# Kernel tuning notes

Hardware: AMD Instinct MI355X
Metric: run time of the kernel (lower is better)

Reference implementation:

```python
import jax, jax.numpy as jnp
import numpy as np

N, D, Z, T, K = 100000, 128, 128, 1024, 256
HID = 512
D_IN = D + 2 * Z  # concat of ctx, z_ctx_pe, z_tgt_pe


def setup_inputs() -> dict:
    key = jax.random.key(0)
    ks = jax.random.split(key, 12)
    inp = {
        'pe': jax.random.normal(ks[0], (N, 4), jnp.float32),
        'context_embedding': jax.random.normal(ks[1], (N, D), jnp.float32),
        'target_embedding': jax.random.normal(ks[2], (N, D), jnp.float32),
        # padded 2-hop subgraph node ids per target (precomputed k_hop_subgraph)
        'sub_nodes': jax.random.randint(ks[3], (T, K), 0, N, jnp.int32),
        'sub_counts': jax.random.randint(ks[4], (T,), 1, K + 1, jnp.int32),
        'target_nodes': jax.random.randint(ks[5], (T,), 0, N, jnp.int32),
        # params
        'z': jax.random.normal(ks[6], (1, Z), jnp.float32) * 0.1,
        'W_pe': jax.random.normal(ks[7], (4, Z), jnp.float32) * 0.5,
        'W1': jax.random.normal(ks[8], (D_IN, HID), jnp.float32) * (1.0 / np.sqrt(D_IN)),
        'b1': jnp.zeros((HID,), jnp.float32),
        'W2': jax.random.normal(ks[9], (HID, D), jnp.float32) * (1.0 / np.sqrt(HID)),
        'b2': jnp.zeros((D,), jnp.float32),
    }
    return inp


def reference(pe, context_embedding, target_embedding, sub_nodes, sub_counts,
              target_nodes, z, W_pe, W1, b1, W2, b2):
    # position_encoding = pe_projector(laplacian_eigenvector_pe)  [N, Z]
    pos_enc = pe @ W_pe
    # gather per-subgraph quantities (batched over T targets, padded to K)
    sub_ctx = context_embedding[sub_nodes]            # [T, K, D]
    z_ctx_pe = z + pos_enc[sub_nodes]                 # [T, K, Z]
    z_tgt_pe = z + pos_enc[target_nodes][:, None, :]  # [T, 1, Z] -> broadcast
    z_tgt_pe = jnp.broadcast_to(z_tgt_pe, z_ctx_pe.shape)
    agg = jnp.concatenate([sub_ctx, z_ctx_pe, z_tgt_pe], axis=-1)  # [T, K, D_IN]
    # predictor MLP
    pred = jax.nn.relu(agg @ W1 + b1) @ W2 + b2       # [T, K, D]
    tgt = target_embedding[target_nodes][:, None, :]  # [T, 1, D]
    sq = (pred - tgt) ** 2                            # [T, K, D]
    counts = jnp.maximum(sub_counts, 1)
    mask = (jnp.arange(K)[None, :] < counts[:, None]).astype(sq.dtype)  # [T, K]
    # per-target MSELoss (mean over n_sub * D elements), summed over targets
    per_target = jnp.sum(sq * mask[:, :, None], axis=(1, 2)) / (counts.astype(sq.dtype) * D)
    return jnp.sum(per_target)
```

## Files before the change

kernel.cpp:

```cpp
#include <hip/hip_runtime.h>
#include <hip/hip_bf16.h>

#define NN   100000
#define DD   128
#define ZZ   128
#define TT   1024
#define KK   256
#define HIDD 512

typedef __attribute__((ext_vector_type(8))) short  short8;
typedef __attribute__((ext_vector_type(4))) float  f32x4;

__device__ inline unsigned short f2bf(float f) {
    union { float f; unsigned int u; } x; x.f = f;
    unsigned int r = x.u + 0x7fffu + ((x.u >> 16) & 1u);
    return (unsigned short)(r >> 16);
}
__device__ inline void load_lds16(const void* g, void* l) {
    __builtin_amdgcn_global_load_lds((const __attribute__((address_space(1))) unsigned int*)g,
                                     (__attribute__((address_space(3))) unsigned int*)l, 16, 0, 0);
}

__global__ __launch_bounds__(256) void prep_tables(
    const float* __restrict__ pe, const float* __restrict__ ctx,
    const float* __restrict__ z, const float* __restrict__ wpe,
    unsigned short* __restrict__ ctx_bf, unsigned short* __restrict__ zpe_bf) {
    int g = blockIdx.x * 256 + threadIdx.x;
    if (g >= NN * 16) return;
    int n = g >> 4, j8 = (g & 15) << 3;
    float p0 = pe[n * 4 + 0], p1 = pe[n * 4 + 1], p2 = pe[n * 4 + 2], p3 = pe[n * 4 + 3];
    float4 c0 = *(const float4*)(ctx + (size_t)n * 128 + j8);
    float4 c1 = *(const float4*)(ctx + (size_t)n * 128 + j8 + 4);
    float4 z0 = *(const float4*)(z + j8);
    float4 z1 = *(const float4*)(z + j8 + 4);
    float4 wa0 = *(const float4*)(wpe + 0 * ZZ + j8), wa1 = *(const float4*)(wpe + 0 * ZZ + j8 + 4);
    float4 wb0 = *(const float4*)(wpe + 1 * ZZ + j8), wb1 = *(const float4*)(wpe + 1 * ZZ + j8 + 4);
    float4 wc0 = *(const float4*)(wpe + 2 * ZZ + j8), wc1 = *(const float4*)(wpe + 2 * ZZ + j8 + 4);
    float4 wd0 = *(const float4*)(wpe + 3 * ZZ + j8), wd1 = *(const float4*)(wpe + 3 * ZZ + j8 + 4);
    float zp[8], cv[8];
    zp[0] = z0.x + p0 * wa0.x + p1 * wb0.x + p2 * wc0.x + p3 * wd0.x;
    zp[1] = z0.y + p0 * wa0.y + p1 * wb0.y + p2 * wc0.y + p3 * wd0.y;
    zp[2] = z0.z + p0 * wa0.z + p1 * wb0.z + p2 * wc0.z + p3 * wd0.z;
    zp[3] = z0.w + p0 * wa0.w + p1 * wb0.w + p2 * wc0.w + p3 * wd0.w;
    zp[4] = z1.x + p0 * wa1.x + p1 * wb1.x + p2 * wc1.x + p3 * wd1.x;
    zp[5] = z1.y + p0 * wa1.y + p1 * wb1.y + p2 * wc1.y + p3 * wd1.y;
    zp[6] = z1.z + p0 * wa1.z + p1 * wb1.z + p2 * wc1.z + p3 * wd1.z;
    zp[7] = z1.w + p0 * wa1.w + p1 * wb1.w + p2 * wc1.w + p3 * wd1.w;
    cv[0] = c0.x; cv[1] = c0.y; cv[2] = c0.z; cv[3] = c0.w;
    cv[4] = c1.x; cv[5] = c1.y; cv[6] = c1.z; cv[7] = c1.w;
    short8 sz, sc;
#pragma unroll
    for (int i = 0; i < 8; ++i) { sz[i] = (short)f2bf(zp[i]); sc[i] = (short)f2bf(cv[i]); }
    *(short8*)(zpe_bf + (size_t)g * 8) = sz;
    *(short8*)(ctx_bf + (size_t)g * 8) = sc;
}

__global__ __launch_bounds__(256) void pack_ct(
    const float* __restrict__ W1, const float* __restrict__ W2,
    const float* __restrict__ pe, const float* __restrict__ z, const float* __restrict__ wpe,
    const int* __restrict__ target_nodes, const float* __restrict__ b1,
    unsigned short* __restrict__ w1p, unsigned short* __restrict__ w2p, float* __restrict__ ct_g) {
    __shared__ float zp[8][128];
    int tid = threadIdx.x;
    if (blockIdx.x < 768) {
        int g = blockIdx.x * 256 + tid;
        if (g < 256 * HIDD) {
            int e = g & 7, l = (g >> 3) & 63, tile = g >> 9;
            int ntg = tile & 7, rem = tile >> 3;
            int kc = rem & 7, hc = rem >> 3;
            int k = kc * 32 + (l >> 4) * 8 + e;
            int n = hc * 128 + ntg * 16 + (l & 15);
            w1p[g] = f2bf(W1[(size_t)k * HIDD + n]);
        } else {
            int q = g - 256 * HIDD;
            int e = q & 7, l = (q >> 3) & 63, tile = q >> 9;
            int ntg = tile & 7, kcg = tile >> 3;
            int k = kcg * 32 + (l >> 4) * 8 + e;
            int n = ntg * 16 + (l & 15);
            w2p[q] = f2bf(W2[(size_t)k * DD + n]);
        }
        return;
    }
    int b = blockIdx.x - 768;
#pragma unroll
    for (int q = 0; q < 4; ++q) {
        int idx = q * 256 + tid;
        int t8 = idx >> 7, zz = idx & 127;
        int tgt = target_nodes[b * 8 + t8];
        zp[t8][zz] = z[zz] + pe[tgt * 4 + 0] * wpe[zz] + pe[tgt * 4 + 1] * wpe[128 + zz]
                           + pe[tgt * 4 + 2] * wpe[256 + zz] + pe[tgt * 4 + 3] * wpe[384 + zz];
    }
    __syncthreads();
    int j0 = tid, j1 = tid + 256;
    float a0[8], a1[8];
    float bb0 = b1[j0], bb1 = b1[j1];
#pragma unroll
    for (int t8 = 0; t8 < 8; ++t8) { a0[t8] = bb0; a1[t8] = bb1; }
#pragma unroll 8
    for (int zz = 0; zz < 128; ++zz) {
        float w0 = W1[(size_t)(256 + zz) * HIDD + j0];
        float w1 = W1[(size_t)(256 + zz) * HIDD + j1];
#pragma unroll
        for (int t8 = 0; t8 < 8; ++t8) { a0[t8] += zp[t8][zz] * w0; a1[t8] += zp[t8][zz] * w1; }
    }
#pragma unroll
    for (int t8 = 0; t8 < 8; ++t8) {
        ct_g[(size_t)(b * 8 + t8) * HIDD + j0] = a0[t8];
        ct_g[(size_t)(b * 8 + t8) * HIDD + j1] = a1[t8];
    }
}

__global__ __launch_bounds__(512) void mp_jepa_main(
    const unsigned short* __restrict__ ctx_bf,
    const unsigned short* __restrict__ zpe_bf,
    const unsigned short* __restrict__ w1p,
    const unsigned short* __restrict__ w2p,
    const float* __restrict__ ct_g,
    const float* __restrict__ target_embedding,
    const int* __restrict__ sub_nodes,
    const int* __restrict__ sub_counts,
    const int* __restrict__ target_nodes,
    const float* __restrict__ b2,
    float* __restrict__ out) {
    const int bid = blockIdx.x;
    const int kt = bid >> 10, t = bid & 1023;
    const int k0 = kt * 64;
    int cnt = sub_counts[t]; if (cnt < 1) cnt = 1;
    if (k0 >= cnt) return;
    const int tgt = target_nodes[t];

    __shared__ __align__(16) unsigned short ctxT[64 * 128];
    __shared__ __align__(16) unsigned short zpeT[64 * 128];
    __shared__ __align__(16) unsigned short hT[64 * 128];
    __shared__ float cts[HIDD];
    __shared__ float tgte[DD];
    __shared__ float b2s[DD];
    __shared__ float red[8];

    const int tid = threadIdx.x;
    const int w = tid >> 6, l = tid & 63;
    const int wm = w & 1, wn = w >> 1;
    const int lo = l & 15, hi = l >> 4;

    {
        const char* cc = (const char*)ctx_bf;
        const char* zc = (const char*)zpe_bf;
        const int base = t * KK + k0;
#pragma unroll
        for (int it = 0; it < 2; ++it) {
            int rgrp = it * 32 + (w << 2);
            int row  = rgrp + hi;
            int node = sub_nodes[base + row];
            int soff = (lo << 4) ^ ((row & 7) << 4);
            load_lds16(cc + (size_t)node * 256 + soff, (char*)ctxT + rgrp * 256);
            load_lds16(zc + (size_t)node * 256 + soff, (char*)zpeT + rgrp * 256);
        }
    }
    if (tid < 128) {
        tgte[tid] = target_embedding[(size_t)tgt * 128 + tid];
        b2s[tid]  = b2[tid];
    }
    cts[tid] = ct_g[(size_t)t * HIDD + tid];
    __syncthreads();

    const short8* w1v = (const short8*)w1p;
    const short8* w2v = (const short8*)w2p;

    f32x4 accP[2][2];
#pragma unroll
    for (int rg = 0; rg < 2; ++rg)
#pragma unroll
        for (int nt = 0; nt < 2; ++nt) accP[rg][nt] = (f32x4){0.f, 0.f, 0.f, 0.f};

    for (int hc = 0; hc < 4; ++hc) {
        f32x4 acc1[2][2];
#pragma unroll
        for (int nt = 0; nt < 2; ++nt) {
            f32x4 cv = *(const f32x4*)&cts[(hc << 7) + (((wn << 1) + nt) << 4) + (hi << 2)];
            acc1[0][nt] = cv;
            acc1[1][nt] = cv;
        }
#pragma unroll
        for (int kc = 0; kc < 8; ++kc) {
            short8 bf0 = w1v[((((hc << 3) + kc) << 3) + (wn << 1) + 0) * 64 + l];
            short8 bf1 = w1v[((((hc << 3) + kc) << 3) + (wn << 1) + 1) * 64 + l];
            const unsigned short* src = (kc < 4) ? ctxT : zpeT;
            int cb = ((kc & 3) << 6) + (hi << 4);
            short8 a[2];
#pragma unroll
            for (int rg = 0; rg < 2; ++rg) {
                int row = (wm << 5) + (rg << 4) + lo;
                a[rg] = *(const short8*)(src + ((row * 256 + (cb ^ ((row & 7) << 4))) >> 1));
            }
#pragma unroll
            for (int rg = 0; rg < 2; ++rg) {
                acc1[rg][0] = __builtin_amdgcn_mfma_f32_16x16x32_bf16(bf0, a[rg], acc1[rg][0], 0, 0, 0);
                acc1[rg][1] = __builtin_amdgcn_mfma_f32_16x16x32_bf16(bf1, a[rg], acc1[rg][1], 0, 0, 0);
            }
        }

        __syncthreads();
#pragma unroll
        for (int nt = 0; nt < 2; ++nt) {
            int cbase = (((wn << 1) + nt) << 5) + (hi << 3);
#pragma unroll
            for (int rg = 0; rg < 2; ++rg) {
                int row = (wm << 5) + (rg << 4) + lo;
                f32x4 v = acc1[rg][nt];
                float v0 = v[0] > 0.f ? v[0] : 0.f;
                float v1 = v[1] > 0.f ? v[1] : 0.f;
                float v2 = v[2] > 0.f ? v[2] : 0.f;
                float v3 = v[3] > 0.f ? v[3] : 0.f;
                uint2 p;
                p.x = (unsigned int)f2bf(v0) | ((unsigned int)f2bf(v1) << 16);
                p.y = (unsigned int)f2bf(v2) | ((unsigned int)f2bf(v3) << 16);
                *(uint2*)((char*)hT + row * 256 + (cbase ^ ((row & 7) << 4))) = p;
            }
        }
        __syncthreads();

#pragma unroll
        for (int kc2 = 0; kc2 < 4; ++kc2) {
            short8 bg0 = w2v[((((hc << 2) + kc2) << 3) + (wn << 1) + 0) * 64 + l];
            short8 bg1 = w2v[((((hc << 2) + kc2) << 3) + (wn << 1) + 1) * 64 + l];
            int cb = (kc2 << 6) + (hi << 4);
#pragma unroll
            for (int rg = 0; rg < 2; ++rg) {
                int row = (wm << 5) + (rg << 4) + lo;
                short8 a = *(const short8*)(hT + ((row * 256 + (cb ^ ((row & 7) << 4))) >> 1));
                accP[rg][0] = __builtin_amdgcn_mfma_f32_16x16x32_bf16(a, bg0, accP[rg][0], 0, 0, 0);
                accP[rg][1] = __builtin_amdgcn_mfma_f32_16x16x32_bf16(a, bg1, accP[rg][1], 0, 0, 0);
            }
        }
    }

    float s = 0.f;
#pragma unroll
    for (int nt = 0; nt < 2; ++nt) {
        int col = (((wn << 1) + nt) << 4) + lo;
        float bb = b2s[col] - tgte[col];
#pragma unroll
        for (int rg = 0; rg < 2; ++rg) {
#pragma unroll
            for (int r = 0; r < 4; ++r) {
                int row = (wm << 5) + (rg << 4) + (hi << 2) + r;
                float d = accP[rg][nt][r] + bb;
                if (k0 + row < cnt) s += d * d;
            }
        }
    }
#pragma unroll
    for (int off = 32; off > 0; off >>= 1) s += __shfl_xor(s, off, 64);
    if (l == 0) red[w] = s;
    __syncthreads();
    if (tid == 0) {
        float tot = (red[0] + red[1] + red[2] + red[3] + red[4] + red[5] + red[6] + red[7])
                    / ((float)cnt * 128.0f);
        atomicAdd(out, tot);
    }
}

extern "C" void kernel_launch(void* const* d_in, const int* in_sizes, int n_in,
                              void* d_out, int out_size, void* d_ws, size_t ws_size,
                              hipStream_t stream) {
    const float* pe           = (const float*)d_in[0];
    const float* ctx          = (const float*)d_in[1];
    const float* tgt_emb      = (const float*)d_in[2];
    const int*   sub_nodes    = (const int*)d_in[3];
    const int*   sub_counts   = (const int*)d_in[4];
    const int*   target_nodes = (const int*)d_in[5];
    const float* z            = (const float*)d_in[6];
    const float* wpe          = (const float*)d_in[7];
    const float* W1           = (const float*)d_in[8];
    const float* b1           = (const float*)d_in[9];
    const float* W2           = (const float*)d_in[10];
    const float* b2           = (const float*)d_in[11];
    float* out = (float*)d_out;

    char* ws = (char*)d_ws;
    unsigned short* ctx_bf = (unsigned short*)ws;
    unsigned short* zpe_bf = (unsigned short*)(ws + 25600000);
    unsigned short* w1p    = (unsigned short*)(ws + 51200000);
    unsigned short* w2p    = (unsigned short*)(ws + 51200000 + 262144);
    float*          ct_g   = (float*)(ws + 51200000 + 262144 + 131072);

    hipMemsetAsync(d_out, 0, sizeof(float), stream);
    prep_tables<<<(NN * 16 + 255) / 256, 256, 0, stream>>>(pe, ctx, z, wpe, ctx_bf, zpe_bf);
    pack_ct<<<896, 256, 0, stream>>>(W1, W2, pe, z, wpe, target_nodes, b1, w1p, w2p, ct_g);
    mp_jepa_main<<<TT * 4, 512, 0, stream>>>(ctx_bf, zpe_bf, w1p, w2p, ct_g, tgt_emb,
                                             sub_nodes, sub_counts, target_nodes, b2, out);
}
```

Measured before the change: 248.9 us.

## Fold PE projection into W1 to drop the zpe table and its gather

Because the context positional encoding is linear in pe (z + pe·W_pe), its contribution to the first layer is rewritten as pe·(W_pe·W1_mid) plus a per-target constant z·W1_mid folded into ct. The change removes the 25.6MB bf16 zpe table from prep_tables along with its per-subgraph gather into LDS, and cuts the first GEMM's K from 256 to 128 plus one zero-padded MFMA over the 4 pe components. This lowers memory traffic in both the prep kernel and the main kernel. In exchange, the precomputed W_pe·W1 product is rounded to bf16 and pe is rounded to bf16, which changes numerical rounding.

```diff
diff --git a/kernel.cpp b/kernel.cpp
--- a/kernel.cpp
+++ b/kernel.cpp
@@ -22,36 +22,16 @@
 }
 
 __global__ __launch_bounds__(256) void prep_tables(
-    const float* __restrict__ pe, const float* __restrict__ ctx,
-    const float* __restrict__ z, const float* __restrict__ wpe,
-    unsigned short* __restrict__ ctx_bf, unsigned short* __restrict__ zpe_bf) {
+    const float* __restrict__ ctx, unsigned short* __restrict__ ctx_bf) {
     int g = blockIdx.x * 256 + threadIdx.x;
     if (g >= NN * 16) return;
-    int n = g >> 4, j8 = (g & 15) << 3;
-    float p0 = pe[n * 4 + 0], p1 = pe[n * 4 + 1], p2 = pe[n * 4 + 2], p3 = pe[n * 4 + 3];
-    float4 c0 = *(const float4*)(ctx + (size_t)n * 128 + j8);
-    float4 c1 = *(const float4*)(ctx + (size_t)n * 128 + j8 + 4);
-    float4 z0 = *(const float4*)(z + j8);
-    float4 z1 = *(const float4*)(z + j8 + 4);
-    float4 wa0 = *(const float4*)(wpe + 0 * ZZ + j8), wa1 = *(const float4*)(wpe + 0 * ZZ + j8 + 4);
-    float4 wb0 = *(const float4*)(wpe + 1 * ZZ + j8), wb1 = *(const float4*)(wpe + 1 * ZZ + j8 + 4);
-    float4 wc0 = *(const float4*)(wpe + 2 * ZZ + j8), wc1 = *(const float4*)(wpe + 2 * ZZ + j8 + 4);
-    float4 wd0 = *(const float4*)(wpe + 3 * ZZ + j8), wd1 = *(const float4*)(wpe + 3 * ZZ + j8 + 4);
-    float zp[8], cv[8];
-    zp[0] = z0.x + p0 * wa0.x + p1 * wb0.x + p2 * wc0.x + p3 * wd0.x;
-    zp[1] = z0.y + p0 * wa0.y + p1 * wb0.y + p2 * wc0.y + p3 * wd0.y;
-    zp[2] = z0.z + p0 * wa0.z + p1 * wb0.z + p2 * wc0.z + p3 * wd0.z;
-    zp[3] = z0.w + p0 * wa0.w + p1 * wb0.w + p2 * wc0.w + p3 * wd0.w;
-    zp[4] = z1.x + p0 * wa1.x + p1 * wb1.x + p2 * wc1.x + p3 * wd1.x;
-    zp[5] = z1.y + p0 * wa1.y + p1 * wb1.y + p2 * wc1.y + p3 * wd1.y;
-    zp[6] = z1.z + p0 * wa1.z + p1 * wb1.z + p2 * wc1.z + p3 * wd1.z;
-    zp[7] = z1.w + p0 * wa1.w + p1 * wb1.w + p2 * wc1.w + p3 * wd1.w;
-    cv[0] = c0.x; cv[1] = c0.y; cv[2] = c0.z; cv[3] = c0.w;
-    cv[4] = c1.x; cv[5] = c1.y; cv[6] = c1.z; cv[7] = c1.w;
-    short8 sz, sc;
-#pragma unroll
-    for (int i = 0; i < 8; ++i) { sz[i] = (short)f2bf(zp[i]); sc[i] = (short)f2bf(cv[i]); }
-    *(short8*)(zpe_bf + (size_t)g * 8) = sz;
+    float4 c0 = *(const float4*)(ctx + (size_t)g * 8);
+    float4 c1 = *(const float4*)(ctx + (size_t)g * 8 + 4);
+    short8 sc;
+    sc[0] = (short)f2bf(c0.x); sc[1] = (short)f2bf(c0.y);
+    sc[2] = (short)f2bf(c0.z); sc[3] = (short)f2bf(c0.w);
+    sc[4] = (short)f2bf(c1.x); sc[5] = (short)f2bf(c1.y);
+    sc[6] = (short)f2bf(c1.z); sc[7] = (short)f2bf(c1.w);
     *(short8*)(ctx_bf + (size_t)g * 8) = sc;
 }
 
@@ -59,64 +39,82 @@
     const float* __restrict__ W1, const float* __restrict__ W2,
     const float* __restrict__ pe, const float* __restrict__ z, const float* __restrict__ wpe,
     const int* __restrict__ target_nodes, const float* __restrict__ b1,
-    unsigned short* __restrict__ w1p, unsigned short* __restrict__ w2p, float* __restrict__ ct_g) {
+    unsigned short* __restrict__ w1p, unsigned short* __restrict__ w2p,
+    unsigned short* __restrict__ w1pe, float* __restrict__ ct_g) {
     __shared__ float zp[8][128];
     int tid = threadIdx.x;
-    if (blockIdx.x < 768) {
-        int g = blockIdx.x * 256 + tid;
-        if (g < 256 * HIDD) {
-            int e = g & 7, l = (g >> 3) & 63, tile = g >> 9;
-            int ntg = tile & 7, rem = tile >> 3;
-            int kc = rem & 7, hc = rem >> 3;
-            int k = kc * 32 + (l >> 4) * 8 + e;
-            int n = hc * 128 + ntg * 16 + (l & 15);
-            w1p[g] = f2bf(W1[(size_t)k * HIDD + n]);
-        } else {
-            int q = g - 256 * HIDD;
-            int e = q & 7, l = (q >> 3) & 63, tile = q >> 9;
-            int ntg = tile & 7, kcg = tile >> 3;
-            int k = kcg * 32 + (l >> 4) * 8 + e;
-            int n = ntg * 16 + (l & 15);
-            w2p[q] = f2bf(W2[(size_t)k * DD + n]);
-        }
+    int b = blockIdx.x;
+    if (b < 256) {
+        int g = b * 256 + tid;
+        int e = g & 7, l = (g >> 3) & 63, tile = g >> 9;
+        int ntg = tile & 7, rem = tile >> 3;
+        int kc = rem & 3, hc = rem >> 2;
+        int k = kc * 32 + (l >> 4) * 8 + e;
+        int n = hc * 128 + ntg * 16 + (l & 15);
+        w1p[g] = f2bf(W1[(size_t)k * HIDD + n]);
         return;
     }
-    int b = blockIdx.x - 768;
-#pragma unroll
-    for (int q = 0; q < 4; ++q) {
-        int idx = q * 256 + tid;
-        int t8 = idx >> 7, zz = idx & 127;
-        int tgt = target_nodes[b * 8 + t8];
-        zp[t8][zz] = z[zz] + pe[tgt * 4 + 0] * wpe[zz] + pe[tgt * 4 + 1] * wpe[128 + zz]
-                           + pe[tgt * 4 + 2] * wpe[256 + zz] + pe[tgt * 4 + 3] * wpe[384 + zz];
-    }
-    __syncthreads();
-    int j0 = tid, j1 = tid + 256;
-    float a0[8], a1[8];
-    float bb0 = b1[j0], bb1 = b1[j1];
-#pragma unroll
-    for (int t8 = 0; t8 < 8; ++t8) { a0[t8] = bb0; a1[t8] = bb1; }
+    if (b < 512) {
+        int q = (b - 256) * 256 + tid;
+        int e = q & 7, l = (q >> 3) & 63, tile = q >> 9;
+        int ntg = tile & 7, kcg = tile >> 3;
+        int k = kcg * 32 + (l >> 4) * 8 + e;
+        int n = ntg * 16 + (l & 15);
+        w2p[q] = f2bf(W2[(size_t)k * DD + n]);
+        return;
+    }
+    if (b < 640) {
+        int bb = b - 512;
+#pragma unroll
+        for (int q = 0; q < 4; ++q) {
+            int idx = q * 256 + tid;
+            int t8 = idx >> 7, zz = idx & 127;
+            int tgt = target_nodes[bb * 8 + t8];
+            zp[t8][zz] = z[zz] + pe[tgt * 4 + 0] * wpe[zz] + pe[tgt * 4 + 1] * wpe[128 + zz]
+                               + pe[tgt * 4 + 2] * wpe[256 + zz] + pe[tgt * 4 + 3] * wpe[384 + zz];
+        }
+        __syncthreads();
+        int j0 = tid, j1 = tid + 256;
+        float a0[8], a1[8];
+        float zb0 = b1[j0], zb1v = b1[j1];
+#pragma unroll
+        for (int t8 = 0; t8 < 8; ++t8) { a0[t8] = 0.f; a1[t8] = 0.f; }
 #pragma unroll 8
-    for (int zz = 0; zz < 128; ++zz) {
-        float w0 = W1[(size_t)(256 + zz) * HIDD + j0];
-        float w1 = W1[(size_t)(256 + zz) * HIDD + j1];
-#pragma unroll
-        for (int t8 = 0; t8 < 8; ++t8) { a0[t8] += zp[t8][zz] * w0; a1[t8] += zp[t8][zz] * w1; }
-    }
-#pragma unroll
-    for (int t8 = 0; t8 < 8; ++t8) {
-        ct_g[(size_t)(b * 8 + t8) * HIDD + j0] = a0[t8];
-        ct_g[(size_t)(b * 8 + t8) * HIDD + j1] = a1[t8];
-    }
+        for (int zz = 0; zz < 128; ++zz) {
+            float zv  = z[zz];
+            float wb0 = W1[(size_t)(128 + zz) * HIDD + j0];
+            float wb1 = W1[(size_t)(128 + zz) * HIDD + j1];
+            float wc0 = W1[(size_t)(256 + zz) * HIDD + j0];
+            float wc1 = W1[(size_t)(256 + zz) * HIDD + j1];
+            zb0 += zv * wb0; zb1v += zv * wb1;
+#pragma unroll
+            for (int t8 = 0; t8 < 8; ++t8) { a0[t8] += zp[t8][zz] * wc0; a1[t8] += zp[t8][zz] * wc1; }
+        }
+#pragma unroll
+        for (int t8 = 0; t8 < 8; ++t8) {
+            ct_g[(size_t)(bb * 8 + t8) * HIDD + j0] = a0[t8] + zb0;
+            ct_g[(size_t)(bb * 8 + t8) * HIDD + j1] = a1[t8] + zb1v;
+        }
+        return;
+    }
+    int idx = b - 640;
+    int j = idx >> 1, half = idx & 1;
+    int col = half * 256 + tid;
+    float acc = 0.f;
+#pragma unroll 8
+    for (int k2 = 0; k2 < 128; ++k2) acc += wpe[j * 128 + k2] * W1[(size_t)(128 + k2) * HIDD + col];
+    int hc = col >> 7, ntg = (col >> 4) & 7, lo2 = col & 15;
+    w1pe[(((hc * 8 + ntg) * 16) + lo2) * 4 + j] = f2bf(acc);
 }
 
 __global__ __launch_bounds__(512) void mp_jepa_main(
     const unsigned short* __restrict__ ctx_bf,
-    const unsigned short* __restrict__ zpe_bf,
     const unsigned short* __restrict__ w1p,
     const unsigned short* __restrict__ w2p,
+    const unsigned short* __restrict__ w1pe,
     const float* __restrict__ ct_g,
     const float* __restrict__ target_embedding,
+    const float* __restrict__ pe,
     const int* __restrict__ sub_nodes,
     const int* __restrict__ sub_counts,
     const int* __restrict__ target_nodes,
@@ -130,9 +128,9 @@
     const int tgt = target_nodes[t];
 
     __shared__ __align__(16) unsigned short ctxT[64 * 128];
-    __shared__ __align__(16) unsigned short zpeT[64 * 128];
     __shared__ __align__(16) unsigned short hT[64 * 128];
-    __shared__ float cts[HIDD];
+    __shared__ __align__(16) unsigned short peT[64 * 4];
+    __shared__ __align__(16) float cts[HIDD];
     __shared__ float tgte[DD];
     __shared__ float b2s[DD];
     __shared__ float red[8];
@@ -141,11 +139,10 @@
     const int w = tid >> 6, l = tid & 63;
     const int wm = w & 1, wn = w >> 1;
     const int lo = l & 15, hi = l >> 4;
+    const int base = t * KK + k0;
 
     {
         const char* cc = (const char*)ctx_bf;
-        const char* zc = (const char*)zpe_bf;
-        const int base = t * KK + k0;
 #pragma unroll
         for (int it = 0; it < 2; ++it) {
             int rgrp = it * 32 + (w << 2);
@@ -153,8 +150,13 @@
             int node = sub_nodes[base + row];
             int soff = (lo << 4) ^ ((row & 7) << 4);
             load_lds16(cc + (size_t)node * 256 + soff, (char*)ctxT + rgrp * 256);
-            load_lds16(zc + (size_t)node * 256 + soff, (char*)zpeT + rgrp * 256);
-        }
+        }
+    }
+    if (tid < 64) {
+        int node = sub_nodes[base + tid];
+        float4 pv = *(const float4*)(pe + (size_t)node * 4);
+        peT[tid * 4 + 0] = f2bf(pv.x); peT[tid * 4 + 1] = f2bf(pv.y);
+        peT[tid * 4 + 2] = f2bf(pv.z); peT[tid * 4 + 3] = f2bf(pv.w);
     }
     if (tid < 128) {
         tgte[tid] = target_embedding[(size_t)tgt * 128 + tid];
@@ -181,21 +183,41 @@
             acc1[1][nt] = cv;
         }
 #pragma unroll
-        for (int kc = 0; kc < 8; ++kc) {
-            short8 bf0 = w1v[((((hc << 3) + kc) << 3) + (wn << 1) + 0) * 64 + l];
-            short8 bf1 = w1v[((((hc << 3) + kc) << 3) + (wn << 1) + 1) * 64 + l];
-            const unsigned short* src = (kc < 4) ? ctxT : zpeT;
-            int cb = ((kc & 3) << 6) + (hi << 4);
+        for (int kc = 0; kc < 4; ++kc) {
+            short8 bf0 = w1v[((((hc << 2) + kc) << 3) + (wn << 1) + 0) * 64 + l];
+            short8 bf1 = w1v[((((hc << 2) + kc) << 3) + (wn << 1) + 1) * 64 + l];
+            int cb = (kc << 6) + (hi << 4);
             short8 a[2];
 #pragma unroll
             for (int rg = 0; rg < 2; ++rg) {
                 int row = (wm << 5) + (rg << 4) + lo;
-                a[rg] = *(const short8*)(src + ((row * 256 + (cb ^ ((row & 7) << 4))) >> 1));
+                a[rg] = *(const short8*)(ctxT + ((row * 256 + (cb ^ ((row & 7) << 4))) >> 1));
             }
 #pragma unroll
             for (int rg = 0; rg < 2; ++rg) {
                 acc1[rg][0] = __builtin_amdgcn_mfma_f32_16x16x32_bf16(bf0, a[rg], acc1[rg][0], 0, 0, 0);
                 acc1[rg][1] = __builtin_amdgcn_mfma_f32_16x16x32_bf16(bf1, a[rg], acc1[rg][1], 0, 0, 0);
+            }
+        }
+        {
+            short8 wf[2];
+#pragma unroll
+            for (int nt = 0; nt < 2; ++nt) {
+                unsigned long long wv = 0ull;
+                if (hi == 0)
+                    wv = *(const unsigned long long*)(w1pe + (((((hc << 3) + (wn << 1) + nt) << 4) + lo) << 2));
+                wf[nt] = (short8){(short)wv, (short)(wv >> 16), (short)(wv >> 32), (short)(wv >> 48),
+                                  0, 0, 0, 0};
+            }
+#pragma unroll
+            for (int rg = 0; rg < 2; ++rg) {
+                int row = (wm << 5) + (rg << 4) + lo;
+                unsigned long long pv = 0ull;
+                if (hi == 0) pv = *(const unsigned long long*)(peT + (row << 2));
+                short8 ap = (short8){(short)pv, (short)(pv >> 16), (short)(pv >> 32), (short)(pv >> 48),
+                                     0, 0, 0, 0};
+                acc1[rg][0] = __builtin_amdgcn_mfma_f32_16x16x32_bf16(wf[0], ap, acc1[rg][0], 0, 0, 0);
+                acc1[rg][1] = __builtin_amdgcn_mfma_f32_16x16x32_bf16(wf[1], ap, acc1[rg][1], 0, 0, 0);
             }
         }
 
@@ -279,14 +301,14 @@
 
     char* ws = (char*)d_ws;
     unsigned short* ctx_bf = (unsigned short*)ws;
-    unsigned short* zpe_bf = (unsigned short*)(ws + 25600000);
-    unsigned short* w1p    = (unsigned short*)(ws + 51200000);
-    unsigned short* w2p    = (unsigned short*)(ws + 51200000 + 262144);
-    float*          ct_g   = (float*)(ws + 51200000 + 262144 + 131072);
+    unsigned short* w1p    = (unsigned short*)(ws + 25600000);
+    unsigned short* w2p    = (unsigned short*)(ws + 25600000 + 131072);
+    unsigned short* w1pe   = (unsigned short*)(ws + 25600000 + 262144);
+    float*          ct_g   = (float*)(ws + 25600000 + 262144 + 4096);
 
     hipMemsetAsync(d_out, 0, sizeof(float), stream);
-    prep_tables<<<(NN * 16 + 255) / 256, 256, 0, stream>>>(pe, ctx, z, wpe, ctx_bf, zpe_bf);
-    pack_ct<<<896, 256, 0, stream>>>(W1, W2, pe, z, wpe, target_nodes, b1, w1p, w2p, ct_g);
-    mp_jepa_main<<<TT * 4, 512, 0, stream>>>(ctx_bf, zpe_bf, w1p, w2p, ct_g, tgt_emb,
+    prep_tables<<<(NN * 16 + 255) / 256, 256, 0, stream>>>(ctx, ctx_bf);
+    pack_ct<<<648, 256, 0, stream>>>(W1, W2, pe, z, wpe, target_nodes, b1, w1p, w2p, w1pe, ct_g);
+    mp_jepa_main<<<TT * 4, 512, 0, stream>>>(ctx_bf, w1p, w2p, w1pe, ct_g, tgt_emb, pe,
                                              sub_nodes, sub_counts, target_nodes, b2, out);
 }
```

Result: faster. 242.0 us (-2.8%).
